# Kernel tuning notes

Hardware: AMD Instinct MI355X
Metric: run time of the kernel (lower is better)

The kernel has to match this reference:

```python
import jax, jax.numpy as jnp
import numpy as np

N_NODES = 10000
N_EDGES = 100000
IN_FEATS = 64
OUT_FEATS = 64
N_EDGE_TYPES = 10


def setup_inputs() -> dict:
    key = jax.random.key(0)
    k_feat, k_src, k_dst, k_ord, k_emb = jax.random.split(key, 5)
    feat = jax.random.normal(k_feat, (N_NODES, IN_FEATS), dtype=jnp.float32)
    src = jax.random.randint(k_src, (N_EDGES,), 0, N_NODES, dtype=jnp.int32)
    dst = jax.random.randint(k_dst, (N_EDGES,), 0, N_NODES, dtype=jnp.int32)
    order = jax.random.randint(k_ord, (N_EDGES,), 0, N_EDGE_TYPES, dtype=jnp.int32)
    # xavier-uniform-like init for the relation-weight embedding table
    emb_weight = jax.random.normal(k_emb, (N_EDGE_TYPES, IN_FEATS * OUT_FEATS), dtype=jnp.float32) * 0.02
    bias = jnp.zeros((OUT_FEATS,), dtype=jnp.float32)
    return {"feat": feat, "src": src, "dst": dst, "order": order,
            "emb_weight": emb_weight, "bias": bias}


def reference(feat, src, dst, order, emb_weight, bias):
    n_nodes, in_feats = feat.shape
    out_feats = emb_weight.shape[1] // in_feats
    n_edges = src.shape[0]
    ones_e = jnp.ones((n_edges,), dtype=feat.dtype)

    # norm='both': scale source features by out_degree^{-1/2}
    out_deg = jnp.clip(jax.ops.segment_sum(ones_e, src, num_segments=n_nodes), 1.0)
    feat_n = feat * (out_deg ** -0.5)[:, None]

    # per-edge relation weight gather: [E, out, in]
    w = emb_weight[order].reshape(n_edges, out_feats, in_feats)
    h_src = feat_n[src]                              # [E, in]
    msg = jnp.einsum('eoi,ei->eo', w, h_src)         # [E, out]

    # scatter-sum aggregate to destination nodes
    rst = jax.ops.segment_sum(msg, dst, num_segments=n_nodes)  # [N, out]

    # post-norm by in_degree^{-1/2}
    in_deg = jnp.clip(jax.ops.segment_sum(ones_e, dst, num_segments=n_nodes), 1.0)
    rst = rst * (in_deg ** -0.5)[:, None]
    return rst + bias
```

## Files before the change

### kernel.cpp

```cpp
#include <hip/hip_runtime.h>
#include <stdint.h>


typedef __attribute__((ext_vector_type(8))) short short8;
typedef __attribute__((ext_vector_type(4))) float f32x4;

constexpr int N_NODES = 10000;
constexpr int N_EDGES = 100000;
constexpr int F = 64;
constexpr int R = 10;
constexpr int BLOCK = 256;
constexpr int EPG = 32;
constexpr int CAP = 16384;
constexpr int GPR = CAP / EPG;
constexpr int N_GROUPS = R * GPR;

union U8 { uint32_t u[4]; short8 s; };

__device__ inline uint32_t pk_hi(float x, float y) {
    uint32_t bx = __float_as_uint(x), by = __float_as_uint(y);
    return (bx >> 16) | (by & 0xFFFF0000u);
}
__device__ inline uint32_t pk_lo(float x, float y) {
    uint32_t bx = __float_as_uint(x), by = __float_as_uint(y);
    float lx = x - __uint_as_float(bx & 0xFFFF0000u);
    float ly = y - __uint_as_float(by & 0xFFFF0000u);
    return (__float_as_uint(lx) >> 16) | (__float_as_uint(ly) & 0xFFFF0000u);
}

__global__ void k_count(const int* __restrict__ src, const int* __restrict__ dst,
                        const int* __restrict__ order, const float* __restrict__ emb,
                        const float* __restrict__ bias,
                        int* deg_out, int* deg_in, int* rel_cnt,
                        int2* __restrict__ sd, uint4* __restrict__ wfrag,
                        float4* __restrict__ outv) {
    __shared__ int hist[R], base[R];
    int tid = threadIdx.x;
    int t = blockIdx.x * BLOCK + tid;
    for (int i = t; i < N_NODES * F / 4; i += gridDim.x * BLOCK)
        outv[i] = ((const float4*)bias)[i & 15];
    if (tid < R) hist[tid] = 0;
    __syncthreads();
    int r = -1, lr = 0, s = 0, d = 0;
    if (t < N_EDGES) {
        s = src[t]; d = dst[t];
        atomicAdd(&deg_out[s], 1);
        atomicAdd(&deg_in[d], 1);
        r = order[t];
        lr = atomicAdd(&hist[r], 1);
    }
    __syncthreads();
    if (tid < R) base[tid] = hist[tid] ? atomicAdd(&rel_cnt[tid], hist[tid]) : 0;
    __syncthreads();
    if (t < N_EDGES)
        sd[(size_t)r * CAP + base[r] + lr] = make_int2(s, d);

    if (t < R * 16 * 64) {
        int lane = t & 63, frag = t >> 6;
        int p = frag & 1, ks = (frag >> 1) & 1, tt = (frag >> 2) & 3, rr = frag >> 4;
        int o = 16 * tt + (lane & 15), q = lane >> 4;
        const float* w = emb + (size_t)rr * F * F + (size_t)o * F + 32 * ks + 8 * q;
        float4 f0 = *(const float4*)w;
        float4 f1 = *(const float4*)(w + 4);
        uint4 v;
        if (p == 0) v = make_uint4(pk_hi(f0.x, f0.y), pk_hi(f0.z, f0.w),
                                   pk_hi(f1.x, f1.y), pk_hi(f1.z, f1.w));
        else        v = make_uint4(pk_lo(f0.x, f0.y), pk_lo(f0.z, f0.w),
                                   pk_lo(f1.x, f1.y), pk_lo(f1.z, f1.w));
        wfrag[(size_t)frag * 64 + lane] = v;
    }
}

__device__ inline void mk_afrag(const float* __restrict__ feat,
                                const int* __restrict__ deg_out,
                                int srow, int q,
                                U8& h0, U8& l0, U8& h1, U8& l1) {
    float nr = rsqrtf((float)max(deg_out[srow], 1));
    const float* row = feat + (size_t)srow * F + 8 * q;
    float4 f0 = *(const float4*)row;
    float4 f1 = *(const float4*)(row + 4);
    float4 f2 = *(const float4*)(row + 32);
    float4 f3 = *(const float4*)(row + 36);
    f0.x *= nr; f0.y *= nr; f0.z *= nr; f0.w *= nr;
    f1.x *= nr; f1.y *= nr; f1.z *= nr; f1.w *= nr;
    f2.x *= nr; f2.y *= nr; f2.z *= nr; f2.w *= nr;
    f3.x *= nr; f3.y *= nr; f3.z *= nr; f3.w *= nr;
    h0.u[0] = pk_hi(f0.x, f0.y); h0.u[1] = pk_hi(f0.z, f0.w);
    h0.u[2] = pk_hi(f1.x, f1.y); h0.u[3] = pk_hi(f1.z, f1.w);
    l0.u[0] = pk_lo(f0.x, f0.y); l0.u[1] = pk_lo(f0.z, f0.w);
    l0.u[2] = pk_lo(f1.x, f1.y); l0.u[3] = pk_lo(f1.z, f1.w);
    h1.u[0] = pk_hi(f2.x, f2.y); h1.u[1] = pk_hi(f2.z, f2.w);
    h1.u[2] = pk_hi(f3.x, f3.y); h1.u[3] = pk_hi(f3.z, f3.w);
    l1.u[0] = pk_lo(f2.x, f2.y); l1.u[1] = pk_lo(f2.z, f2.w);
    l1.u[2] = pk_lo(f3.x, f3.y); l1.u[3] = pk_lo(f3.z, f3.w);
}

__global__ __launch_bounds__(BLOCK, 3) void k_edge(
    const float* __restrict__ feat, const int* __restrict__ deg_out,
    const int* __restrict__ deg_in, const short8* __restrict__ wfrag,
    const int* __restrict__ rel_cnt, const int2* __restrict__ sd,
    float* __restrict__ out) {
    int lane = threadIdx.x & 63;
    int wib = threadIdx.x >> 6;
    int g = blockIdx.x * (BLOCK / 64) + wib;
    if (g >= N_GROUPS) return;
    int r = g >> 9;
    int e0 = (g & (GPR - 1)) * EPG;
    int cnt = rel_cnt[r];
    if (e0 >= cnt) return;

    int q = lane >> 4;
    int iA = e0 + (lane & 15), iB = iA + 16;
    const int2* sdr = sd + (size_t)r * CAP;
    int2 mA = iA < cnt ? sdr[iA] : make_int2(0, -1);
    int2 mB = iB < cnt ? sdr[iB] : make_int2(0, -1);

    U8 Ah0, Al0, Ah1, Al1, Bh0, Bl0, Bh1, Bl1;
    mk_afrag(feat, deg_out, mA.x, q, Ah0, Al0, Ah1, Al1);
    mk_afrag(feat, deg_out, mB.x, q, Bh0, Bl0, Bh1, Bl1);

    const short8* wf = wfrag + (size_t)r * 16 * 64;
    f32x4 acc0[4], acc1[4];
#pragma unroll
    for (int t = 0; t < 4; ++t) {
        acc0[t] = (f32x4){0.f, 0.f, 0.f, 0.f};
        acc1[t] = (f32x4){0.f, 0.f, 0.f, 0.f};
    }

#pragma unroll
    for (int t = 0; t < 4; ++t) {
        short8 bh0 = wf[(t * 4 + 0) * 64 + lane];
        short8 bl0 = wf[(t * 4 + 1) * 64 + lane];
        short8 bh1 = wf[(t * 4 + 2) * 64 + lane];
        short8 bl1 = wf[(t * 4 + 3) * 64 + lane];
        f32x4 x = acc0[t], y = acc1[t];
        x = __builtin_amdgcn_mfma_f32_16x16x32_bf16(Al0.s, bh0, x, 0, 0, 0);
        y = __builtin_amdgcn_mfma_f32_16x16x32_bf16(Bl0.s, bh0, y, 0, 0, 0);
        x = __builtin_amdgcn_mfma_f32_16x16x32_bf16(Ah0.s, bl0, x, 0, 0, 0);
        y = __builtin_amdgcn_mfma_f32_16x16x32_bf16(Bh0.s, bl0, y, 0, 0, 0);
        x = __builtin_amdgcn_mfma_f32_16x16x32_bf16(Ah0.s, bh0, x, 0, 0, 0);
        y = __builtin_amdgcn_mfma_f32_16x16x32_bf16(Bh0.s, bh0, y, 0, 0, 0);
        x = __builtin_amdgcn_mfma_f32_16x16x32_bf16(Al1.s, bh1, x, 0, 0, 0);
        y = __builtin_amdgcn_mfma_f32_16x16x32_bf16(Bl1.s, bh1, y, 0, 0, 0);
        x = __builtin_amdgcn_mfma_f32_16x16x32_bf16(Ah1.s, bl1, x, 0, 0, 0);
        y = __builtin_amdgcn_mfma_f32_16x16x32_bf16(Bh1.s, bl1, y, 0, 0, 0);
        x = __builtin_amdgcn_mfma_f32_16x16x32_bf16(Ah1.s, bh1, x, 0, 0, 0);
        y = __builtin_amdgcn_mfma_f32_16x16x32_bf16(Bh1.s, bh1, y, 0, 0, 0);
        acc0[t] = x; acc1[t] = y;
    }

    int col = lane & 15;
#pragma unroll
    for (int gg = 0; gg < 4; ++gg) {
        int row = q * 4 + gg;
        int dA = __shfl(mA.y, row);
        int dB = __shfl(mB.y, row);
        if (dA >= 0) {
            float sc = rsqrtf((float)max(deg_in[dA], 1));
#pragma unroll
            for (int t = 0; t < 4; ++t)
                unsafeAtomicAdd(&out[(size_t)dA * F + 16 * t + col], acc0[t][gg] * sc);
        }
        if (dB >= 0) {
            float sc = rsqrtf((float)max(deg_in[dB], 1));
#pragma unroll
            for (int t = 0; t < 4; ++t)
                unsafeAtomicAdd(&out[(size_t)dB * F + 16 * t + col], acc1[t][gg] * sc);
        }
    }
}

extern "C" void kernel_launch(void* const* d_in, const int* in_sizes, int n_in,
                              void* d_out, int out_size, void* d_ws, size_t ws_size,
                              hipStream_t stream) {
    const float* feat  = (const float*)d_in[0];
    const int*   src   = (const int*)d_in[1];
    const int*   dst   = (const int*)d_in[2];
    const int*   order = (const int*)d_in[3];
    const float* emb   = (const float*)d_in[4];
    const float* bias  = (const float*)d_in[5];
    float* out = (float*)d_out;

    int*   deg_out  = (int*)d_ws;
    int*   deg_in   = deg_out + N_NODES;
    int*   rel_cnt  = deg_in + N_NODES;
    int2*  sd       = (int2*)(rel_cnt + 16);
    uint4* wfrag    = (uint4*)(sd + R * CAP);

    size_t zbytes = (size_t)(2 * N_NODES + 16) * sizeof(int);
    hipMemsetAsync(d_ws, 0, zbytes, stream);

    int eb = (N_EDGES + BLOCK - 1) / BLOCK;
    k_count<<<eb, BLOCK, 0, stream>>>(src, dst, order, emb, bias, deg_out, deg_in,
                                      rel_cnt, sd, wfrag, (float4*)out);
    int gblocks = (N_GROUPS + (BLOCK / 64) - 1) / (BLOCK / 64);
    k_edge<<<gblocks, BLOCK, 0, stream>>>(feat, deg_out, deg_in, (const short8*)wfrag,
                                          rel_cnt, sd, out);
}
```

Before: 106.9 us.

## Fuse memset, count, and edge kernels into one cooperative persistent kernel

Replaces the memset plus two kernel launches with a single cooperative kernel that zeroes counters, initializes the output and weight fragments, bins edges by relation, and then runs the MFMA edge phase, with grid-wide syncs between phases. Blocks loop persistently over edge chunks and edge groups. The goal is to remove launch and inter-kernel gaps. The cost is two grid syncs, fewer blocks than the original edge launch, lower occupancy bounds, and a per-call occupancy query on the host.

```diff
diff --git a/kernel.cpp b/kernel.cpp
--- a/kernel.cpp
+++ b/kernel.cpp
@@ -1,5 +1,8 @@
 #include <hip/hip_runtime.h>
+#include <hip/hip_cooperative_groups.h>
 #include <stdint.h>
+
+namespace cg = cooperative_groups;
 
 
 typedef __attribute__((ext_vector_type(8))) short short8;
@@ -10,6 +13,7 @@
 constexpr int F = 64;
 constexpr int R = 10;
 constexpr int BLOCK = 256;
+constexpr int MAX_BLOCKS = 768;
 constexpr int EPG = 32;
 constexpr int CAP = 16384;
 constexpr int GPR = CAP / EPG;
@@ -26,49 +30,6 @@
     float lx = x - __uint_as_float(bx & 0xFFFF0000u);
     float ly = y - __uint_as_float(by & 0xFFFF0000u);
     return (__float_as_uint(lx) >> 16) | (__float_as_uint(ly) & 0xFFFF0000u);
-}
-
-__global__ void k_count(const int* __restrict__ src, const int* __restrict__ dst,
-                        const int* __restrict__ order, const float* __restrict__ emb,
-                        const float* __restrict__ bias,
-                        int* deg_out, int* deg_in, int* rel_cnt,
-                        int2* __restrict__ sd, uint4* __restrict__ wfrag,
-                        float4* __restrict__ outv) {
-    __shared__ int hist[R], base[R];
-    int tid = threadIdx.x;
-    int t = blockIdx.x * BLOCK + tid;
-    for (int i = t; i < N_NODES * F / 4; i += gridDim.x * BLOCK)
-        outv[i] = ((const float4*)bias)[i & 15];
-    if (tid < R) hist[tid] = 0;
-    __syncthreads();
-    int r = -1, lr = 0, s = 0, d = 0;
-    if (t < N_EDGES) {
-        s = src[t]; d = dst[t];
-        atomicAdd(&deg_out[s], 1);
-        atomicAdd(&deg_in[d], 1);
-        r = order[t];
-        lr = atomicAdd(&hist[r], 1);
-    }
-    __syncthreads();
-    if (tid < R) base[tid] = hist[tid] ? atomicAdd(&rel_cnt[tid], hist[tid]) : 0;
-    __syncthreads();
-    if (t < N_EDGES)
-        sd[(size_t)r * CAP + base[r] + lr] = make_int2(s, d);
-
-    if (t < R * 16 * 64) {
-        int lane = t & 63, frag = t >> 6;
-        int p = frag & 1, ks = (frag >> 1) & 1, tt = (frag >> 2) & 3, rr = frag >> 4;
-        int o = 16 * tt + (lane & 15), q = lane >> 4;
-        const float* w = emb + (size_t)rr * F * F + (size_t)o * F + 32 * ks + 8 * q;
-        float4 f0 = *(const float4*)w;
-        float4 f1 = *(const float4*)(w + 4);
-        uint4 v;
-        if (p == 0) v = make_uint4(pk_hi(f0.x, f0.y), pk_hi(f0.z, f0.w),
-                                   pk_hi(f1.x, f1.y), pk_hi(f1.z, f1.w));
-        else        v = make_uint4(pk_lo(f0.x, f0.y), pk_lo(f0.z, f0.w),
-                                   pk_lo(f1.x, f1.y), pk_lo(f1.z, f1.w));
-        wfrag[(size_t)frag * 64 + lane] = v;
-    }
 }
 
 __device__ inline void mk_afrag(const float* __restrict__ feat,
@@ -95,77 +56,128 @@
     l1.u[2] = pk_lo(f3.x, f3.y); l1.u[3] = pk_lo(f3.z, f3.w);
 }
 
-__global__ __launch_bounds__(BLOCK, 3) void k_edge(
-    const float* __restrict__ feat, const int* __restrict__ deg_out,
-    const int* __restrict__ deg_in, const short8* __restrict__ wfrag,
-    const int* __restrict__ rel_cnt, const int2* __restrict__ sd,
+__global__ __launch_bounds__(BLOCK, 2) void k_all(
+    const float* __restrict__ feat, const int* __restrict__ src,
+    const int* __restrict__ dst, const int* __restrict__ order,
+    const float* __restrict__ emb, const float* __restrict__ bias,
+    int* deg_out, int* deg_in, int* rel_cnt,
+    int2* __restrict__ sd, uint4* __restrict__ wfrag,
     float* __restrict__ out) {
-    int lane = threadIdx.x & 63;
-    int wib = threadIdx.x >> 6;
-    int g = blockIdx.x * (BLOCK / 64) + wib;
-    if (g >= N_GROUPS) return;
-    int r = g >> 9;
-    int e0 = (g & (GPR - 1)) * EPG;
-    int cnt = rel_cnt[r];
-    if (e0 >= cnt) return;
-
+    cg::grid_group grid = cg::this_grid();
+    int tid = threadIdx.x;
+    int t0 = blockIdx.x * BLOCK + tid;
+    int NT = gridDim.x * BLOCK;
+
+    for (int i = t0; i < 2 * N_NODES + 16; i += NT) deg_out[i] = 0;
+    float4* outv = (float4*)out;
+    for (int i = t0; i < N_NODES * F / 4; i += NT)
+        outv[i] = ((const float4*)bias)[i & 15];
+    for (int i = t0; i < R * 16 * 64; i += NT) {
+        int lane = i & 63, frag = i >> 6;
+        int p = frag & 1, ks = (frag >> 1) & 1, tt = (frag >> 2) & 3, rr = frag >> 4;
+        int o = 16 * tt + (lane & 15), q = lane >> 4;
+        const float* w = emb + (size_t)rr * F * F + (size_t)o * F + 32 * ks + 8 * q;
+        float4 f0 = *(const float4*)w;
+        float4 f1 = *(const float4*)(w + 4);
+        uint4 v;
+        if (p == 0) v = make_uint4(pk_hi(f0.x, f0.y), pk_hi(f0.z, f0.w),
+                                   pk_hi(f1.x, f1.y), pk_hi(f1.z, f1.w));
+        else        v = make_uint4(pk_lo(f0.x, f0.y), pk_lo(f0.z, f0.w),
+                                   pk_lo(f1.x, f1.y), pk_lo(f1.z, f1.w));
+        wfrag[(size_t)frag * 64 + lane] = v;
+    }
+    grid.sync();
+
+    __shared__ int hist[R], hbase[R];
+    for (int base = blockIdx.x * BLOCK; base < N_EDGES; base += NT) {
+        int e = base + tid;
+        if (tid < R) hist[tid] = 0;
+        __syncthreads();
+        int r1 = -1, lr = 0, s1 = 0, d1 = 0;
+        if (e < N_EDGES) {
+            s1 = src[e]; d1 = dst[e];
+            atomicAdd(&deg_out[s1], 1);
+            atomicAdd(&deg_in[d1], 1);
+            r1 = order[e];
+            lr = atomicAdd(&hist[r1], 1);
+        }
+        __syncthreads();
+        if (tid < R) hbase[tid] = hist[tid] ? atomicAdd(&rel_cnt[tid], hist[tid]) : 0;
+        __syncthreads();
+        if (e < N_EDGES)
+            sd[(size_t)r1 * CAP + hbase[r1] + lr] = make_int2(s1, d1);
+        __syncthreads();
+    }
+    grid.sync();
+
+    int lane = tid & 63;
+    int slot = blockIdx.x * (BLOCK / 64) + (tid >> 6);
+    int wave_slots = gridDim.x * (BLOCK / 64);
     int q = lane >> 4;
-    int iA = e0 + (lane & 15), iB = iA + 16;
-    const int2* sdr = sd + (size_t)r * CAP;
-    int2 mA = iA < cnt ? sdr[iA] : make_int2(0, -1);
-    int2 mB = iB < cnt ? sdr[iB] : make_int2(0, -1);
-
-    U8 Ah0, Al0, Ah1, Al1, Bh0, Bl0, Bh1, Bl1;
-    mk_afrag(feat, deg_out, mA.x, q, Ah0, Al0, Ah1, Al1);
-    mk_afrag(feat, deg_out, mB.x, q, Bh0, Bl0, Bh1, Bl1);
-
-    const short8* wf = wfrag + (size_t)r * 16 * 64;
-    f32x4 acc0[4], acc1[4];
-#pragma unroll
-    for (int t = 0; t < 4; ++t) {
-        acc0[t] = (f32x4){0.f, 0.f, 0.f, 0.f};
-        acc1[t] = (f32x4){0.f, 0.f, 0.f, 0.f};
-    }
-
-#pragma unroll
-    for (int t = 0; t < 4; ++t) {
-        short8 bh0 = wf[(t * 4 + 0) * 64 + lane];
-        short8 bl0 = wf[(t * 4 + 1) * 64 + lane];
-        short8 bh1 = wf[(t * 4 + 2) * 64 + lane];
-        short8 bl1 = wf[(t * 4 + 3) * 64 + lane];
-        f32x4 x = acc0[t], y = acc1[t];
-        x = __builtin_amdgcn_mfma_f32_16x16x32_bf16(Al0.s, bh0, x, 0, 0, 0);
-        y = __builtin_amdgcn_mfma_f32_16x16x32_bf16(Bl0.s, bh0, y, 0, 0, 0);
-        x = __builtin_amdgcn_mfma_f32_16x16x32_bf16(Ah0.s, bl0, x, 0, 0, 0);
-        y = __builtin_amdgcn_mfma_f32_16x16x32_bf16(Bh0.s, bl0, y, 0, 0, 0);
-        x = __builtin_amdgcn_mfma_f32_16x16x32_bf16(Ah0.s, bh0, x, 0, 0, 0);
-        y = __builtin_amdgcn_mfma_f32_16x16x32_bf16(Bh0.s, bh0, y, 0, 0, 0);
-        x = __builtin_amdgcn_mfma_f32_16x16x32_bf16(Al1.s, bh1, x, 0, 0, 0);
-        y = __builtin_amdgcn_mfma_f32_16x16x32_bf16(Bl1.s, bh1, y, 0, 0, 0);
-        x = __builtin_amdgcn_mfma_f32_16x16x32_bf16(Ah1.s, bl1, x, 0, 0, 0);
-        y = __builtin_amdgcn_mfma_f32_16x16x32_bf16(Bh1.s, bl1, y, 0, 0, 0);
-        x = __builtin_amdgcn_mfma_f32_16x16x32_bf16(Ah1.s, bh1, x, 0, 0, 0);
-        y = __builtin_amdgcn_mfma_f32_16x16x32_bf16(Bh1.s, bh1, y, 0, 0, 0);
-        acc0[t] = x; acc1[t] = y;
-    }
-
     int col = lane & 15;
-#pragma unroll
-    for (int gg = 0; gg < 4; ++gg) {
-        int row = q * 4 + gg;
-        int dA = __shfl(mA.y, row);
-        int dB = __shfl(mB.y, row);
-        if (dA >= 0) {
-            float sc = rsqrtf((float)max(deg_in[dA], 1));
-#pragma unroll
-            for (int t = 0; t < 4; ++t)
-                unsafeAtomicAdd(&out[(size_t)dA * F + 16 * t + col], acc0[t][gg] * sc);
-        }
-        if (dB >= 0) {
-            float sc = rsqrtf((float)max(deg_in[dB], 1));
-#pragma unroll
-            for (int t = 0; t < 4; ++t)
-                unsafeAtomicAdd(&out[(size_t)dB * F + 16 * t + col], acc1[t][gg] * sc);
+    const short8* wfr = (const short8*)wfrag;
+
+    for (int g = slot; g < N_GROUPS; g += wave_slots) {
+        int r = g >> 9;
+        int e0 = (g & (GPR - 1)) * EPG;
+        int cnt = rel_cnt[r];
+        if (e0 >= cnt) continue;
+
+        int iA = e0 + col, iB = iA + 16;
+        const int2* sdr = sd + (size_t)r * CAP;
+        int2 mA = iA < cnt ? sdr[iA] : make_int2(0, -1);
+        int2 mB = iB < cnt ? sdr[iB] : make_int2(0, -1);
+
+        U8 Ah0, Al0, Ah1, Al1, Bh0, Bl0, Bh1, Bl1;
+        mk_afrag(feat, deg_out, mA.x, q, Ah0, Al0, Ah1, Al1);
+        mk_afrag(feat, deg_out, mB.x, q, Bh0, Bl0, Bh1, Bl1);
+
+        const short8* wf = wfr + (size_t)r * 16 * 64;
+        f32x4 acc0[4], acc1[4];
+#pragma unroll
+        for (int tt = 0; tt < 4; ++tt) {
+            acc0[tt] = (f32x4){0.f, 0.f, 0.f, 0.f};
+            acc1[tt] = (f32x4){0.f, 0.f, 0.f, 0.f};
+        }
+#pragma unroll
+        for (int tt = 0; tt < 4; ++tt) {
+            short8 bh0 = wf[(tt * 4 + 0) * 64 + lane];
+            short8 bl0 = wf[(tt * 4 + 1) * 64 + lane];
+            short8 bh1 = wf[(tt * 4 + 2) * 64 + lane];
+            short8 bl1 = wf[(tt * 4 + 3) * 64 + lane];
+            f32x4 x = acc0[tt], y = acc1[tt];
+            x = __builtin_amdgcn_mfma_f32_16x16x32_bf16(Al0.s, bh0, x, 0, 0, 0);
+            y = __builtin_amdgcn_mfma_f32_16x16x32_bf16(Bl0.s, bh0, y, 0, 0, 0);
+            x = __builtin_amdgcn_mfma_f32_16x16x32_bf16(Ah0.s, bl0, x, 0, 0, 0);
+            y = __builtin_amdgcn_mfma_f32_16x16x32_bf16(Bh0.s, bl0, y, 0, 0, 0);
+            x = __builtin_amdgcn_mfma_f32_16x16x32_bf16(Ah0.s, bh0, x, 0, 0, 0);
+            y = __builtin_amdgcn_mfma_f32_16x16x32_bf16(Bh0.s, bh0, y, 0, 0, 0);
+            x = __builtin_amdgcn_mfma_f32_16x16x32_bf16(Al1.s, bh1, x, 0, 0, 0);
+            y = __builtin_amdgcn_mfma_f32_16x16x32_bf16(Bl1.s, bh1, y, 0, 0, 0);
+            x = __builtin_amdgcn_mfma_f32_16x16x32_bf16(Ah1.s, bl1, x, 0, 0, 0);
+            y = __builtin_amdgcn_mfma_f32_16x16x32_bf16(Bh1.s, bl1, y, 0, 0, 0);
+            x = __builtin_amdgcn_mfma_f32_16x16x32_bf16(Ah1.s, bh1, x, 0, 0, 0);
+            y = __builtin_amdgcn_mfma_f32_16x16x32_bf16(Bh1.s, bh1, y, 0, 0, 0);
+            acc0[tt] = x; acc1[tt] = y;
+        }
+
+#pragma unroll
+        for (int rg = 0; rg < 4; ++rg) {
+            int row = q * 4 + rg;
+            int dA = __shfl(mA.y, row);
+            int dB = __shfl(mB.y, row);
+            if (dA >= 0) {
+                float sc = rsqrtf((float)max(deg_in[dA], 1));
+#pragma unroll
+                for (int tt = 0; tt < 4; ++tt)
+                    unsafeAtomicAdd(&out[(size_t)dA * F + 16 * tt + col], acc0[tt][rg] * sc);
+            }
+            if (dB >= 0) {
+                float sc = rsqrtf((float)max(deg_in[dB], 1));
+#pragma unroll
+                for (int tt = 0; tt < 4; ++tt)
+                    unsafeAtomicAdd(&out[(size_t)dB * F + 16 * tt + col], acc1[tt][rg] * sc);
+            }
         }
     }
 }
@@ -187,13 +199,15 @@
     int2*  sd       = (int2*)(rel_cnt + 16);
     uint4* wfrag    = (uint4*)(sd + R * CAP);
 
-    size_t zbytes = (size_t)(2 * N_NODES + 16) * sizeof(int);
-    hipMemsetAsync(d_ws, 0, zbytes, stream);
-
-    int eb = (N_EDGES + BLOCK - 1) / BLOCK;
-    k_count<<<eb, BLOCK, 0, stream>>>(src, dst, order, emb, bias, deg_out, deg_in,
-                                      rel_cnt, sd, wfrag, (float4*)out);
-    int gblocks = (N_GROUPS + (BLOCK / 64) - 1) / (BLOCK / 64);
-    k_edge<<<gblocks, BLOCK, 0, stream>>>(feat, deg_out, deg_in, (const short8*)wfrag,
-                                          rel_cnt, sd, out);
-}
+    int occ = 0;
+    hipOccupancyMaxActiveBlocksPerMultiprocessor(&occ, k_all, BLOCK, 0);
+    if (occ < 1) occ = 1;
+    int blocks = occ * 256;
+    if (blocks > MAX_BLOCKS) blocks = MAX_BLOCKS;
+
+    void* args[] = { (void*)&feat, (void*)&src, (void*)&dst, (void*)&order,
+                     (void*)&emb, (void*)&bias, (void*)&deg_out, (void*)&deg_in,
+                     (void*)&rel_cnt, (void*)&sd, (void*)&wfrag, (void*)&out };
+    hipLaunchCooperativeKernel((void*)k_all, dim3(blocks), dim3(BLOCK),
+                               args, 0, stream);
+}
```

Result: slower. 232.5 us (+117.4%).
